# Performance work log

Measured on AMD Instinct MI355X. Metric: run time of the kernel, lower is better.

Reference implementation:

```python
import jax, jax.numpy as jnp
import numpy as np

N_SPECIES = 2
N_RBF = 16
HIDDEN = 64
CUTOFF = 2.5


def setup_inputs() -> dict:
    key = jax.random.key(0)
    ks = jax.random.split(key, 10)
    B, N = 8, 1024
    positions = jax.random.uniform(ks[0], (B, N, 3), dtype=jnp.float32) * 10.0
    types = jax.random.randint(ks[1], (B, N), 0, N_SPECIES)
    in_dim = N_SPECIES + N_SPECIES * N_RBF  # 34
    def lin(k, fan_in, fan_out):
        bound = 1.0 / np.sqrt(fan_in)
        kw, kb = jax.random.split(k)
        W = jax.random.uniform(kw, (fan_in, fan_out), minval=-bound, maxval=bound, dtype=jnp.float32)
        b = jax.random.uniform(kb, (fan_out,), minval=-bound, maxval=bound, dtype=jnp.float32)
        return W, b
    W1, b1 = lin(ks[2], in_dim, 64)
    W2, b2 = lin(ks[3], 64, 64)
    W3, b3 = lin(ks[4], 64, HIDDEN)
    return {"positions": positions, "types": types,
            "W1": W1, "b1": b1, "W2": W2, "b2": b2, "W3": W3, "b3": b3}


def _forward(positions, types, W1, b1, W2, b2, W3, b3):
    B, N, _ = positions.shape
    # pairwise distances with safe sqrt (zero grad on diagonal, matching torch norm subgradient)
    disp = positions[:, :, None, :] - positions[:, None, :, :]          # [B,N,N,3]
    sq = jnp.sum(disp * disp, axis=-1)                                   # [B,N,N]
    nz = sq > 0.0
    d = jnp.sqrt(jnp.where(nz, sq, 1.0)) * nz
    # RBF expansion
    centers = jnp.linspace(0.0, CUTOFF, N_RBF)
    widths = jnp.full((N_RBF,), CUTOFF / max(N_RBF - 1, 1))
    diff = d[..., None] - centers                                        # [B,N,N,R]
    rbf = jnp.exp(-(diff ** 2) / (widths ** 2 + 1e-12))
    # smooth polynomial cutoff
    x = d / CUTOFF
    cut = jnp.where(d < CUTOFF, 1.0 - 6.0 * x ** 5 + 15.0 * x ** 4 - 10.0 * x ** 3, 0.0)
    rbf = rbf * cut[..., None]
    eye = jnp.eye(N, dtype=bool)[None, :, :, None]
    rbf = jnp.where(eye, 0.0, rbf)
    # species-weighted neighbor aggregation
    onehot = jax.nn.one_hot(types, N_SPECIES, dtype=positions.dtype)      # [B,N,S]
    env = jnp.einsum('bijr,bjs->birs', rbf, onehot).reshape(B, N, -1)     # [B,N,R*S]
    feats = jnp.concatenate([onehot, env], axis=-1)                       # [B,N,S+S*R]
    h = jax.nn.silu(feats @ W1 + b1)
    h = jax.nn.silu(h @ W2 + b2)
    return h @ W3 + b3                                                    # [B,N,HIDDEN]


def reference(positions, types, W1, b1, W2, b2, W3, b3):
    return _forward(positions, types, W1, b1, W2, b2, W3, b3)
```

## Files before the change

### kernel.cpp

```cpp
#include <hip/hip_runtime.h>
#include <hip/hip_bf16.h>

#define NTHREADS 256
#define N_ATOMS  1024
#define HIDDEN   64
#define SEGCAP   512

__global__ __launch_bounds__(NTHREADS) void LocalFeatureEncoder_40063454937486_kernel(
    const float* __restrict__ pos,
    const int*   __restrict__ types,
    const float* __restrict__ W1,
    const float* __restrict__ b1,
    const float* __restrict__ W2,
    const float* __restrict__ b2,
    const float* __restrict__ W3,
    const float* __restrict__ b3,
    float*       __restrict__ out)
{
    const int tid  = threadIdx.x;
    const int lane = tid & 63;
    const int wav  = tid >> 6;
    const int a    = blockIdx.x * 4 + wav;
    const int bidx = blockIdx.x >> 8;
    const int i    = a & (N_ATOMS - 1);

    __shared__ float4 sp[N_ATOMS];
    __shared__ float  qv[4 * SEGCAP];

    const float* pf   = pos + (size_t)bidx * (N_ATOMS * 3);
    const int*   typb = types + (size_t)bidx * N_ATOMS;

    {
        const float4 p0 = *(const float4*)(pf + tid * 12);
        const float4 p1 = *(const float4*)(pf + tid * 12 + 4);
        const float4 p2 = *(const float4*)(pf + tid * 12 + 8);
        const int4   tv = *(const int4*)(typb + tid * 4);

        const float px[4] = {p0.x, p0.w, p1.z, p2.y};
        const float py[4] = {p0.y, p1.x, p1.w, p2.z};
        const float pz[4] = {p0.z, p1.y, p2.x, p2.w};
        const int   tj[4] = {tv.x, tv.y, tv.z, tv.w};
#pragma unroll
        for (int q = 0; q < 4; ++q) {
            sp[tid * 4 + q] = make_float4(px[q], py[q], pz[q],
                                          (tj[q] == 0) ? 1.0f : -1.0f);
        }
    }
    __syncthreads();

    const float4 self = sp[i];
    const float xi = self.x, yi = self.y, zi = self.z;

    float* seg = &qv[wav * SEGCAP];
    int base = 0;
#pragma unroll
    for (int s = 0; s < N_ATOMS / 64; ++s) {
        const int j = lane + s * 64;
        const float4 nb = sp[j];
        const float dx = xi - nb.x;
        const float dy = yi - nb.y;
        const float dz = zi - nb.z;
        const float sq = dx * dx + dy * dy + dz * dz;
        const bool pred = (j != i) && (sq < 6.25f);

        const unsigned long long mask = __ballot(pred);
        if (pred) {
            const float d = sqrtf(sq);
            const int idx = base + (int)__popcll(mask & ((1ull << lane) - 1ull));
            seg[idx] = (nb.w > 0.0f) ? d : -d;
        }
        base += (int)__popcll(mask);
    }
    const int npad = (base + 3) & ~3;
    if (lane < npad - base) seg[base + lane] = 100.0f;
    __syncthreads();

    float acc0 = 0.0f, acc1 = 0.0f;
    {
        const int   slot = lane >> 4;
        const int   r    = lane & 15;
        const float c    = (float)r * (2.5f / 15.0f);
        for (int e = slot; e < npad; e += 4) {
            const float v   = seg[e];
            const float d   = fabsf(v);
            const float x   = d * 0.4f;
            const float x3  = x * x * x;
            const float cutv = 1.0f + x3 * (-10.0f + x * (15.0f - 6.0f * x));
            const float diff = d - c;
            const float ex   = __expf(diff * diff * -36.0f);
            const float m0 = (v > 0.0f) ? cutv : 0.0f;
            const float m1 = (v > 0.0f) ? 0.0f : cutv;
            acc0 += ex * m0;
            acc1 += ex * m1;
        }
    }
    acc0 += __shfl_xor(acc0, 16, 64);
    acc0 += __shfl_xor(acc0, 32, 64);
    acc1 += __shfl_xor(acc1, 16, 64);
    acc1 += __shfl_xor(acc1, 32, 64);

    const int t  = lane;
    const int ti = (self.w < 0.0f) ? 1 : 0;

    float h1 = b1[t] + W1[ti * HIDDEN + t];
#pragma unroll
    for (int r = 0; r < 16; ++r) {
        h1 += __shfl(acc0, r, 64) * W1[(2 + 2 * r + 0) * HIDDEN + t];
        h1 += __shfl(acc1, r, 64) * W1[(2 + 2 * r + 1) * HIDDEN + t];
    }
    h1 = h1 / (1.0f + __expf(-h1));

    float h2 = b2[t];
#pragma unroll
    for (int k = 0; k < HIDDEN; ++k) {
        h2 += __shfl(h1, k, 64) * W2[k * HIDDEN + t];
    }
    h2 = h2 / (1.0f + __expf(-h2));

    float o = b3[t];
#pragma unroll
    for (int k = 0; k < HIDDEN; ++k) {
        o += __shfl(h2, k, 64) * W3[k * HIDDEN + t];
    }
    out[(size_t)a * HIDDEN + t] = o;
}

extern "C" void kernel_launch(void* const* d_in, const int* in_sizes, int n_in,
                              void* d_out, int out_size, void* d_ws, size_t ws_size,
                              hipStream_t stream) {
    const float* pos   = (const float*)d_in[0];
    const int*   types = (const int*)d_in[1];
    const float* W1    = (const float*)d_in[2];
    const float* b1    = (const float*)d_in[3];
    const float* W2    = (const float*)d_in[4];
    const float* b2    = (const float*)d_in[5];
    const float* W3    = (const float*)d_in[6];
    const float* b3    = (const float*)d_in[7];
    float*       out   = (float*)d_out;

    const int BN = in_sizes[1];

    LocalFeatureEncoder_40063454937486_kernel<<<BN / 4, NTHREADS, 0, stream>>>(
        pos, types, W1, b1, W2, b2, W3, b3, out);
}
```

Baseline: 89.41 us.

## Stage MLP weights in shared memory and process eight atoms per block

Blocks grow from 256 to 512 threads, so each block handles eight atoms instead of four. All of W1, W2 and W3 (about 41 KB) are copied into LDS once per block, and the three MLP layers read weights from LDS instead of global memory. The intent is to share the weight and position loads across more waves and to avoid repeated global/L1 weight fetches. In exchange, LDS use per block rises to roughly 63 KB, which limits resident blocks per CU, and the per-wave neighbor buffer shrinks to 192 entries, which could overflow if an atom has more neighbors inside the cutoff.

Measured after the change: 96.15 us. 1.08x slower.

```diff
diff --git a/kernel.cpp b/kernel.cpp
--- a/kernel.cpp
+++ b/kernel.cpp
@@ -1,10 +1,13 @@
 #include <hip/hip_runtime.h>
 #include <hip/hip_bf16.h>
 
-#define NTHREADS 256
+#define NTHREADS 512
 #define N_ATOMS  1024
 #define HIDDEN   64
-#define SEGCAP   512
+#define SEGCAP   192
+#define W2OFF    2176
+#define W3OFF    6272
+#define WTOT     10368
 
 __global__ __launch_bounds__(NTHREADS) void LocalFeatureEncoder_40063454937486_kernel(
     const float* __restrict__ pos,
@@ -20,17 +23,18 @@
     const int tid  = threadIdx.x;
     const int lane = tid & 63;
     const int wav  = tid >> 6;
-    const int a    = blockIdx.x * 4 + wav;
-    const int bidx = blockIdx.x >> 8;
+    const int a    = blockIdx.x * 8 + wav;
+    const int bidx = blockIdx.x >> 7;
     const int i    = a & (N_ATOMS - 1);
 
     __shared__ float4 sp[N_ATOMS];
-    __shared__ float  qv[4 * SEGCAP];
+    __shared__ float  sw[WTOT];
+    __shared__ float  qv[8 * SEGCAP];
 
     const float* pf   = pos + (size_t)bidx * (N_ATOMS * 3);
     const int*   typb = types + (size_t)bidx * N_ATOMS;
 
-    {
+    if (tid < 256) {
         const float4 p0 = *(const float4*)(pf + tid * 12);
         const float4 p1 = *(const float4*)(pf + tid * 12 + 4);
         const float4 p2 = *(const float4*)(pf + tid * 12 + 8);
@@ -41,9 +45,16 @@
         const float pz[4] = {p0.z, p1.y, p2.x, p2.w};
         const int   tj[4] = {tv.x, tv.y, tv.z, tv.w};
 #pragma unroll
-        for (int q = 0; q < 4; ++q) {
+        for (int q = 0; q < 4; ++q)
             sp[tid * 4 + q] = make_float4(px[q], py[q], pz[q],
                                           (tj[q] == 0) ? 1.0f : -1.0f);
+    }
+    {
+        for (int v = tid; v < 544; v += NTHREADS)
+            *(float4*)&sw[v * 4] = *(const float4*)(W1 + v * 4);
+        for (int v = tid; v < 1024; v += NTHREADS) {
+            *(float4*)&sw[W2OFF + v * 4] = *(const float4*)(W2 + v * 4);
+            *(float4*)&sw[W3OFF + v * 4] = *(const float4*)(W3 + v * 4);
         }
     }
     __syncthreads();
@@ -88,10 +99,8 @@
             const float cutv = 1.0f + x3 * (-10.0f + x * (15.0f - 6.0f * x));
             const float diff = d - c;
             const float ex   = __expf(diff * diff * -36.0f);
-            const float m0 = (v > 0.0f) ? cutv : 0.0f;
-            const float m1 = (v > 0.0f) ? 0.0f : cutv;
-            acc0 += ex * m0;
-            acc1 += ex * m1;
+            acc0 += ex * ((v > 0.0f) ? cutv : 0.0f);
+            acc1 += ex * ((v > 0.0f) ? 0.0f : cutv);
         }
     }
     acc0 += __shfl_xor(acc0, 16, 64);
@@ -102,26 +111,24 @@
     const int t  = lane;
     const int ti = (self.w < 0.0f) ? 1 : 0;
 
-    float h1 = b1[t] + W1[ti * HIDDEN + t];
+    float h1 = b1[t] + sw[ti * HIDDEN + t];
 #pragma unroll
     for (int r = 0; r < 16; ++r) {
-        h1 += __shfl(acc0, r, 64) * W1[(2 + 2 * r + 0) * HIDDEN + t];
-        h1 += __shfl(acc1, r, 64) * W1[(2 + 2 * r + 1) * HIDDEN + t];
+        h1 += __shfl(acc0, r, 64) * sw[(2 + 2 * r + 0) * HIDDEN + t];
+        h1 += __shfl(acc1, r, 64) * sw[(2 + 2 * r + 1) * HIDDEN + t];
     }
     h1 = h1 / (1.0f + __expf(-h1));
 
     float h2 = b2[t];
 #pragma unroll
-    for (int k = 0; k < HIDDEN; ++k) {
-        h2 += __shfl(h1, k, 64) * W2[k * HIDDEN + t];
-    }
+    for (int k = 0; k < HIDDEN; ++k)
+        h2 += __shfl(h1, k, 64) * sw[W2OFF + k * HIDDEN + t];
     h2 = h2 / (1.0f + __expf(-h2));
 
     float o = b3[t];
 #pragma unroll
-    for (int k = 0; k < HIDDEN; ++k) {
-        o += __shfl(h2, k, 64) * W3[k * HIDDEN + t];
-    }
+    for (int k = 0; k < HIDDEN; ++k)
+        o += __shfl(h2, k, 64) * sw[W3OFF + k * HIDDEN + t];
     out[(size_t)a * HIDDEN + t] = o;
 }
 
@@ -140,6 +147,6 @@
 
     const int BN = in_sizes[1];
 
-    LocalFeatureEncoder_40063454937486_kernel<<<BN / 4, NTHREADS, 0, stream>>>(
+    LocalFeatureEncoder_40063454937486_kernel<<<BN / 8, NTHREADS, 0, stream>>>(
         pos, types, W1, b1, W2, b2, W3, b3, out);
 }
```
